# Kernel optimization log

Measured on AMD Instinct MI355X. Metric: run time of the kernel, lower is better.

## Reference

```python
import jax, jax.numpy as jnp
import numpy as np

K = 1024          # num_embeddings
D = 128           # embedding_dim
COMMITMENT_COST = 0.25


def setup_inputs() -> dict:
    key = jax.random.key(0)
    k1, k2 = jax.random.split(key)
    inputs = jax.random.normal(k1, (16, D, 4096), dtype=jnp.float32)
    codebook = jax.random.normal(k2, (K, D), dtype=jnp.float32)
    return {"inputs": inputs, "codebook": codebook}


def reference(inputs, codebook):
    # inputs: [B, D, T]; codebook: [K, D]
    B, Dd, T = inputs.shape
    flat = jnp.transpose(inputs, (0, 2, 1)).reshape(-1, Dd)  # [N, D], N = B*T
    N = flat.shape[0]

    d = (jnp.sum(flat * flat, axis=1, keepdims=True)
         + jnp.sum(codebook * codebook, axis=1)
         - 2.0 * flat @ codebook.T)
    idx = jnp.argmin(d, axis=1)  # [N]

    # gather-based quantization (same math as one-hot @ codebook)
    quantized = codebook[idx]                                   # [N, D]
    quantized = quantized.reshape(B, T, Dd).transpose(0, 2, 1)  # [B, D, T]

    # commitment loss (quantized detached; stop_gradient irrelevant in fwd)
    e_latent_loss = jnp.mean((jax.lax.stop_gradient(quantized) - inputs) ** 2)
    loss = COMMITMENT_COST * e_latent_loss

    # straight-through estimator
    quantized_st = inputs + jax.lax.stop_gradient(quantized - inputs)

    # perplexity from code usage histogram (= mean of one-hot encodings)
    counts = jnp.zeros((codebook.shape[0],), dtype=jnp.float32).at[idx].add(1.0)
    avg_probs = counts / N
    perplexity = jnp.exp(-jnp.sum(avg_probs * jnp.log(avg_probs + 1e-10)))

    return loss, quantized_st, perplexity, idx.reshape(B, T)
```

## Files before the change

### kernel.cpp

```cpp
#include <hip/hip_runtime.h>

#define T_FULL 4096
#define D 128
#define K 1024
#define NVEC 65536
#define BDT 8388608
#define BT 128
#define NBLK (NVEC / BT)
#define KT 64
#define NIT (K / KT)
#define PLANE_B (K * D * 2)
#define TILE_B (2 * KT * D * 2)

typedef _Float16 f16x8 __attribute__((ext_vector_type(8)));
typedef float f32x4 __attribute__((ext_vector_type(4)));

#define MFMA(a, b, c) __builtin_amdgcn_mfma_f32_16x16x32_f16((a), (b), (c), 0, 0, 0)

#define GLOAD_LDS(g, l)                                                        \
  __builtin_amdgcn_global_load_lds(                                            \
      (const __attribute__((address_space(1))) unsigned int*)(g),              \
      (__attribute__((address_space(3))) unsigned int*)(l), 16, 0, 0)

__global__ __launch_bounds__(128) void prep_kernel(const float* __restrict__ cb,
    float* __restrict__ ee, _Float16* __restrict__ E1, _Float16* __restrict__ E2,
    unsigned int* __restrict__ counts, unsigned int* __restrict__ done,
    float* __restrict__ loss_acc) {
  int k = blockIdx.x, d = threadIdx.x;
  if (d == 0) {
    counts[k] = 0u;
    if (k == 0) { *done = 0u; *loss_acc = 0.f; }
  }
  float e = cb[k * D + d];
  float v = e * e;
#pragma unroll
  for (int o = 32; o > 0; o >>= 1) v += __shfl_down(v, o, 64);
  __shared__ float tmp[2];
  if ((d & 63) == 0) tmp[d >> 6] = v;
  __syncthreads();
  if (d == 0) ee[k] = tmp[0] + tmp[1];

  float s = 2.0f * e;
  _Float16 h1 = (_Float16)s;
  _Float16 h2 = (_Float16)(s - (float)h1);
  E1[k * D + d] = h1;
  E2[k * D + d] = h2;
}

__global__ __launch_bounds__(256, 2) void vq_main(
    const float* __restrict__ inp, const float* __restrict__ cb,
    const float* __restrict__ ee, const _Float16* __restrict__ Eplanes,
    unsigned int* __restrict__ counts, unsigned int* __restrict__ done,
    float* __restrict__ loss_acc, float* __restrict__ out) {
  __shared__ __align__(16) _Float16 Bs[2 * 2 * KT * D];
  __shared__ float ee_sh[K];
  __shared__ int   midx[BT];
  __shared__ float lred[4];
  __shared__ int   lastf;

  float* out_q   = out + 1;
  float* out_idx = out + 2 + BDT;

  const int tid  = threadIdx.x;
  const int lane = tid & 63;
  const int w    = tid >> 6;
  const int c    = lane & 15;
  const int q    = lane >> 4;
  const int b    = blockIdx.x >> 5;
  const int t0   = (blockIdx.x & 31) * BT;

  unsigned soff[8], slds[8];
#pragma unroll
  for (int i = 0; i < 8; ++i) {
    int flat = tid + i * 256;
    int p    = flat >> 10;
    int s    = flat & 1023;
    int code = s >> 4;
    int dgp  = s & 15;
    int dg   = dgp ^ (code & 15);
    soff[i] = (unsigned)(p * PLANE_B + code * 256 + dg * 16);
    slds[i] = (unsigned)(flat * 16);
  }
  const char* Eb = (const char*)Eplanes;

#pragma unroll
  for (int i = 0; i < 8; ++i)
    GLOAD_LDS(Eb + soff[i], (char*)Bs + slds[i]);

  f16x8 A1[2][4], A2[2][4];
  {
    const float* xin = inp + (size_t)b * D * T_FULL + t0 + w * 32 + c;
#pragma unroll
    for (int n = 0; n < 2; ++n)
#pragma unroll
      for (int dc = 0; dc < 4; ++dc) {
        f16x8 a1, a2;
#pragma unroll
        for (int j = 0; j < 8; ++j) {
          int d = dc * 32 + q * 8 + j;
          float x = xin[(size_t)d * T_FULL + n * 16];
          _Float16 h1 = (_Float16)x;
          _Float16 h2 = (_Float16)(x - (float)h1);
          a1[j] = h1; a2[j] = h2;
        }
        A1[n][dc] = a1; A2[n][dc] = a2;
      }
  }
#pragma unroll
  for (int i = tid; i < K; i += 256) ee_sh[i] = ee[i];
  __syncthreads();

  float bv[2][4];
  int   bi[2][4];
#pragma unroll
  for (int n = 0; n < 2; ++n)
#pragma unroll
    for (int r = 0; r < 4; ++r) { bv[n][r] = 3.4e38f; bi[n][r] = 0; }

  for (int it = 0; it < NIT; ++it) {
    const int kt = it * KT;
    const int bb = it & 1;

    if (it) __syncthreads();

    if (it != NIT - 1) {
      const int ktn = kt + KT;
      const unsigned lbo = (unsigned)((bb ^ 1) * TILE_B);
#pragma unroll
      for (int i = 0; i < 8; ++i)
        GLOAD_LDS(Eb + (size_t)ktn * 256 + soff[i], (char*)Bs + lbo + slds[i]);
    }

    f32x4 acc[2][4];
#pragma unroll
    for (int n = 0; n < 2; ++n)
#pragma unroll
      for (int kf = 0; kf < 4; ++kf) acc[n][kf] = (f32x4){0.f, 0.f, 0.f, 0.f};

    const char* Bp = (const char*)Bs + bb * TILE_B;
#pragma unroll
    for (int dc = 0; dc < 4; ++dc) {
      const int sw = ((dc * 4 + q) ^ c) * 16;
      f16x8 B1[4], B2[4];
#pragma unroll
      for (int kf = 0; kf < 4; ++kf) {
        const int ro = (kf * 16 + c) * 256 + sw;
        B1[kf] = *(const f16x8*)(Bp + ro);
        B2[kf] = *(const f16x8*)(Bp + 16384 + ro);
      }
#pragma unroll
      for (int n = 0; n < 2; ++n)
#pragma unroll
        for (int kf = 0; kf < 4; ++kf) {
          f32x4 a = acc[n][kf];
          a = MFMA(A1[n][dc], B1[kf], a);
          a = MFMA(A1[n][dc], B2[kf], a);
          a = MFMA(A2[n][dc], B1[kf], a);
          acc[n][kf] = a;
        }
    }

#pragma unroll
    for (int kf = 0; kf < 4; ++kf) {
      const int code = kt + kf * 16 + c;
      const float eev = ee_sh[code];
#pragma unroll
      for (int n = 0; n < 2; ++n)
#pragma unroll
        for (int r = 0; r < 4; ++r) {
          float dist = eev - acc[n][kf][r];
          if (dist < bv[n][r]) { bv[n][r] = dist; bi[n][r] = code; }
        }
    }
  }

#pragma unroll
  for (int m = 1; m <= 8; m <<= 1)
#pragma unroll
    for (int n = 0; n < 2; ++n)
#pragma unroll
      for (int r = 0; r < 4; ++r) {
        float ov = __shfl_xor(bv[n][r], m, 64);
        int   oi = __shfl_xor(bi[n][r], m, 64);
        if (ov < bv[n][r] || (ov == bv[n][r] && oi < bi[n][r])) {
          bv[n][r] = ov; bi[n][r] = oi;
        }
      }
  if (c == 0) {
#pragma unroll
    for (int n = 0; n < 2; ++n)
#pragma unroll
      for (int r = 0; r < 4; ++r)
        midx[w * 32 + n * 16 + q * 4 + r] = bi[n][r];
  }
  __syncthreads();

  if (tid < BT) {
    int ki = midx[tid];
    out_idx[(size_t)b * T_FULL + t0 + tid] = (float)ki;
    atomicAdd(&counts[ki], 1u);
  }

  float lsum = 0.f;
  {
    const int t  = tid & 127;
    const int dh = tid >> 7;
    const int kq = midx[t];
    const float* crow = cb + (size_t)kq * D + dh * 64;
    const float* xrow = inp + ((size_t)b * D + dh * 64) * T_FULL + t0 + t;
    float*       qrow = out_q + ((size_t)b * D + dh * 64) * T_FULL + t0 + t;
#pragma unroll
    for (int dd = 0; dd < 64; dd += 4) {
      float4 qv = *(const float4*)(crow + dd);
      float x0 = xrow[(size_t)(dd + 0) * T_FULL];
      float x1 = xrow[(size_t)(dd + 1) * T_FULL];
      float x2 = xrow[(size_t)(dd + 2) * T_FULL];
      float x3 = xrow[(size_t)(dd + 3) * T_FULL];
      float df;
      df = qv.x - x0; lsum = fmaf(df, df, lsum); qrow[(size_t)(dd + 0) * T_FULL] = qv.x;
      df = qv.y - x1; lsum = fmaf(df, df, lsum); qrow[(size_t)(dd + 1) * T_FULL] = qv.y;
      df = qv.z - x2; lsum = fmaf(df, df, lsum); qrow[(size_t)(dd + 2) * T_FULL] = qv.z;
      df = qv.w - x3; lsum = fmaf(df, df, lsum); qrow[(size_t)(dd + 3) * T_FULL] = qv.w;
    }
  }
#pragma unroll
  for (int o = 32; o > 0; o >>= 1) lsum += __shfl_down(lsum, o, 64);
  if (lane == 0) lred[w] = lsum;
  __syncthreads();
  if (tid == 0) {
    atomicAdd(loss_acc, lred[0] + lred[1] + lred[2] + lred[3]);
    __threadfence();
    unsigned ticket = atomicAdd(done, 1u);
    lastf = (ticket == NBLK - 1) ? 1 : 0;
  }
  __syncthreads();

  if (lastf) {
    __threadfence();
    float ent = 0.f;
#pragma unroll
    for (int i = tid; i < K; i += 256) {
      float cnt = (float)atomicAdd(&counts[i], 0u);
      float p = cnt * (1.0f / (float)NVEC);
      ent = fmaf(p, logf(p + 1e-10f), ent);
    }
#pragma unroll
    for (int o = 32; o > 0; o >>= 1) ent += __shfl_down(ent, o, 64);
    if (lane == 0) lred[w] = ent;
    __syncthreads();
    if (tid == 0) {
      float e = lred[0] + lred[1] + lred[2] + lred[3];
      float l = atomicAdd(loss_acc, 0.f);
      out[0]       = 0.25f * (l / (float)BDT);
      out[1 + BDT] = expf(-e);
    }
  }
}

extern "C" void kernel_launch(void* const* d_in, const int* in_sizes, int n_in,
                              void* d_out, int out_size, void* d_ws, size_t ws_size,
                              hipStream_t stream) {
  const float* inp = (const float*)d_in[0];
  const float* cb  = (const float*)d_in[1];
  float* out = (float*)d_out;

  char* ws = (char*)d_ws;
  unsigned int* counts  = (unsigned int*)ws;
  unsigned int* done    = (unsigned int*)(ws + 4096);
  float*        lossacc = (float*)(ws + 4160);
  float*        ee      = (float*)(ws + 8192);
  _Float16*     E1      = (_Float16*)(ws + 12288);
  _Float16*     E2      = (_Float16*)(ws + 12288 + PLANE_B);

  prep_kernel<<<K, 128, 0, stream>>>(cb, ee, E1, E2, counts, done, lossacc);
  vq_main<<<NBLK, 256, 0, stream>>>(inp, cb, ee, E1, counts, done, lossacc, out);
}
```

Baseline: 182.8 us.

## Split codebook across wave pairs with smaller token tile for higher occupancy

Halves the token tile per block to 64 and the codebook tile to 32, and splits the codebook tile between two waves per token group so each wave computes one 16-code fragment instead of four. Partial argmins from the two wave halves are merged through shared memory before the gather and loss stage. The goal is lower register and LDS pressure (launch bounds raised to 4 blocks per CU) and more blocks to fill the GPU. The cost is that each block's codebook loads now feed only 64 tokens, so codebook traffic per token doubles, and there are twice as many loop iterations with a barrier each.

```diff
diff --git a/kernel.cpp b/kernel.cpp
--- a/kernel.cpp
+++ b/kernel.cpp
@@ -5,9 +5,9 @@
 #define K 1024
 #define NVEC 65536
 #define BDT 8388608
-#define BT 128
+#define BT 64
 #define NBLK (NVEC / BT)
-#define KT 64
+#define KT 32
 #define NIT (K / KT)
 #define PLANE_B (K * D * 2)
 #define TILE_B (2 * KT * D * 2)
@@ -47,14 +47,16 @@
   E2[k * D + d] = h2;
 }
 
-__global__ __launch_bounds__(256, 2) void vq_main(
+__global__ __launch_bounds__(256, 4) void vq_main(
     const float* __restrict__ inp, const float* __restrict__ cb,
     const float* __restrict__ ee, const _Float16* __restrict__ Eplanes,
     unsigned int* __restrict__ counts, unsigned int* __restrict__ done,
     float* __restrict__ loss_acc, float* __restrict__ out) {
   __shared__ __align__(16) _Float16 Bs[2 * 2 * KT * D];
   __shared__ float ee_sh[K];
-  __shared__ int   midx[BT];
+  __shared__ float mval[2][BT];
+  __shared__ int   midx[2][BT];
+  __shared__ int   fidx[BT];
   __shared__ float lred[4];
   __shared__ int   lastf;
 
@@ -64,17 +66,19 @@
   const int tid  = threadIdx.x;
   const int lane = tid & 63;
   const int w    = tid >> 6;
+  const int wn   = w >> 1;
+  const int wk   = w & 1;
   const int c    = lane & 15;
   const int q    = lane >> 4;
-  const int b    = blockIdx.x >> 5;
-  const int t0   = (blockIdx.x & 31) * BT;
-
-  unsigned soff[8], slds[8];
-#pragma unroll
-  for (int i = 0; i < 8; ++i) {
+  const int b    = blockIdx.x >> 6;
+  const int t0   = (blockIdx.x & 63) * BT;
+
+  unsigned soff[4], slds[4];
+#pragma unroll
+  for (int i = 0; i < 4; ++i) {
     int flat = tid + i * 256;
-    int p    = flat >> 10;
-    int s    = flat & 1023;
+    int p    = flat >> 9;
+    int s    = flat & 511;
     int code = s >> 4;
     int dgp  = s & 15;
     int dg   = dgp ^ (code & 15);
@@ -84,12 +88,12 @@
   const char* Eb = (const char*)Eplanes;
 
 #pragma unroll
-  for (int i = 0; i < 8; ++i)
+  for (int i = 0; i < 4; ++i)
     GLOAD_LDS(Eb + soff[i], (char*)Bs + slds[i]);
 
   f16x8 A1[2][4], A2[2][4];
   {
-    const float* xin = inp + (size_t)b * D * T_FULL + t0 + w * 32 + c;
+    const float* xin = inp + (size_t)b * D * T_FULL + t0 + wn * 32 + c;
 #pragma unroll
     for (int n = 0; n < 2; ++n)
 #pragma unroll
@@ -127,48 +131,38 @@
       const int ktn = kt + KT;
       const unsigned lbo = (unsigned)((bb ^ 1) * TILE_B);
 #pragma unroll
-      for (int i = 0; i < 8; ++i)
+      for (int i = 0; i < 4; ++i)
         GLOAD_LDS(Eb + (size_t)ktn * 256 + soff[i], (char*)Bs + lbo + slds[i]);
     }
 
-    f32x4 acc[2][4];
-#pragma unroll
-    for (int n = 0; n < 2; ++n)
-#pragma unroll
-      for (int kf = 0; kf < 4; ++kf) acc[n][kf] = (f32x4){0.f, 0.f, 0.f, 0.f};
+    f32x4 acc[2];
+#pragma unroll
+    for (int n = 0; n < 2; ++n) acc[n] = (f32x4){0.f, 0.f, 0.f, 0.f};
 
     const char* Bp = (const char*)Bs + bb * TILE_B;
 #pragma unroll
     for (int dc = 0; dc < 4; ++dc) {
-      const int sw = ((dc * 4 + q) ^ c) * 16;
-      f16x8 B1[4], B2[4];
-#pragma unroll
-      for (int kf = 0; kf < 4; ++kf) {
-        const int ro = (kf * 16 + c) * 256 + sw;
-        B1[kf] = *(const f16x8*)(Bp + ro);
-        B2[kf] = *(const f16x8*)(Bp + 16384 + ro);
-      }
+      const int ro = (wk * 16 + c) * 256 + ((dc * 4 + q) ^ c) * 16;
+      f16x8 B1 = *(const f16x8*)(Bp + ro);
+      f16x8 B2 = *(const f16x8*)(Bp + 8192 + ro);
+#pragma unroll
+      for (int n = 0; n < 2; ++n) {
+        f32x4 a = acc[n];
+        a = MFMA(A1[n][dc], B1, a);
+        a = MFMA(A1[n][dc], B2, a);
+        a = MFMA(A2[n][dc], B1, a);
+        acc[n] = a;
+      }
+    }
+
+    {
+      const int code = kt + wk * 16 + c;
+      const float eev = ee_sh[code];
 #pragma unroll
       for (int n = 0; n < 2; ++n)
 #pragma unroll
-        for (int kf = 0; kf < 4; ++kf) {
-          f32x4 a = acc[n][kf];
-          a = MFMA(A1[n][dc], B1[kf], a);
-          a = MFMA(A1[n][dc], B2[kf], a);
-          a = MFMA(A2[n][dc], B1[kf], a);
-          acc[n][kf] = a;
-        }
-    }
-
-#pragma unroll
-    for (int kf = 0; kf < 4; ++kf) {
-      const int code = kt + kf * 16 + c;
-      const float eev = ee_sh[code];
-#pragma unroll
-      for (int n = 0; n < 2; ++n)
-#pragma unroll
         for (int r = 0; r < 4; ++r) {
-          float dist = eev - acc[n][kf][r];
+          float dist = eev - acc[n][r];
           if (dist < bv[n][r]) { bv[n][r] = dist; bi[n][r] = code; }
         }
     }
@@ -190,27 +184,34 @@
 #pragma unroll
     for (int n = 0; n < 2; ++n)
 #pragma unroll
-      for (int r = 0; r < 4; ++r)
-        midx[w * 32 + n * 16 + q * 4 + r] = bi[n][r];
+      for (int r = 0; r < 4; ++r) {
+        const int t_loc = wn * 32 + n * 16 + q * 4 + r;
+        mval[wk][t_loc] = bv[n][r];
+        midx[wk][t_loc] = bi[n][r];
+      }
   }
   __syncthreads();
 
   if (tid < BT) {
-    int ki = midx[tid];
+    float v0 = mval[0][tid], v1 = mval[1][tid];
+    int   i0 = midx[0][tid], i1 = midx[1][tid];
+    int ki = (v1 < v0 || (v1 == v0 && i1 < i0)) ? i1 : i0;
+    fidx[tid] = ki;
     out_idx[(size_t)b * T_FULL + t0 + tid] = (float)ki;
     atomicAdd(&counts[ki], 1u);
   }
+  __syncthreads();
 
   float lsum = 0.f;
   {
-    const int t  = tid & 127;
-    const int dh = tid >> 7;
-    const int kq = midx[t];
-    const float* crow = cb + (size_t)kq * D + dh * 64;
-    const float* xrow = inp + ((size_t)b * D + dh * 64) * T_FULL + t0 + t;
-    float*       qrow = out_q + ((size_t)b * D + dh * 64) * T_FULL + t0 + t;
-#pragma unroll
-    for (int dd = 0; dd < 64; dd += 4) {
+    const int t  = tid & 63;
+    const int dh = tid >> 6;
+    const int kq = fidx[t];
+    const float* crow = cb + (size_t)kq * D + dh * 32;
+    const float* xrow = inp + ((size_t)b * D + dh * 32) * T_FULL + t0 + t;
+    float*       qrow = out_q + ((size_t)b * D + dh * 32) * T_FULL + t0 + t;
+#pragma unroll
+    for (int dd = 0; dd < 32; dd += 4) {
       float4 qv = *(const float4*)(crow + dd);
       float x0 = xrow[(size_t)(dd + 0) * T_FULL];
       float x1 = xrow[(size_t)(dd + 1) * T_FULL];
```

After: 204.6 us. +12.0%, slower.
